# Kernel optimization log

Hardware: AMD Instinct MI355X
Metric: run time of the kernel (lower is better)

The kernel has to match this reference:

```python
import jax, jax.numpy as jnp
import numpy as np

B, D, H, O, E, K = 16384, 3072, 128, 10, 8, 2


def setup_inputs() -> dict:
    key = jax.random.key(0)
    ks = jax.random.split(key, 9)
    s_d = 1.0 / np.sqrt(D)
    s_h = 1.0 / np.sqrt(H)
    return {
        "x": jax.random.normal(ks[0], (B, D), dtype=jnp.float32),
        "gate_w": jax.random.uniform(ks[1], (D, E), jnp.float32, -s_d, s_d),
        "gate_b": jnp.zeros((E,), jnp.float32),
        "w1": jax.random.uniform(ks[2], (E, D, H), jnp.float32, -s_d, s_d),
        "b1": jax.random.uniform(ks[3], (E, H), jnp.float32, -s_d, s_d),
        "w2": jax.random.uniform(ks[4], (E, H, H), jnp.float32, -s_h, s_h),
        "b2": jax.random.uniform(ks[5], (E, H), jnp.float32, -s_h, s_h),
        "w3": jax.random.uniform(ks[6], (E, H, O), jnp.float32, -s_h, s_h),
        "b3": jax.random.uniform(ks[7], (E, O), jnp.float32, -s_h, s_h),
    }


def reference(x, gate_w, gate_b, w1, b1, w2, b2, w3, b3):
    # Gate: scores [B, E]
    scores = x @ gate_w + gate_b
    _, topk_idx = jax.lax.top_k(scores, K)          # [B, K]
    mask = jax.nn.one_hot(topk_idx, E, dtype=scores.dtype).sum(axis=-2)  # [B, E] 0/1
    weights = jax.nn.softmax(scores, axis=-1) * mask
    weights = weights / (weights.sum(axis=-1, keepdims=True) + 1e-8)

    # Compute all experts (dropout is identity in eval mode)
    h1 = jax.nn.relu(jnp.einsum('bd,edh->beh', x, w1) + b1)   # [B, E, H]
    h2 = jax.nn.relu(jnp.einsum('beh,ehg->beg', h1, w2) + b2)  # [B, E, H]
    out = jnp.einsum('beh,eho->beo', h2, w3) + b3              # [B, E, O]

    y = jnp.einsum('be,beo->bo', weights, out)                 # [B, O]
    return y
```

## Files before the change

### kernel.cpp

```cpp
#include <hip/hip_runtime.h>
#include <hip/hip_bf16.h>

#define B_ROWS 16384
#define D_DIM  3072
#define H_DIM  128
#define O_DIM  10
#define E_NUM  8

typedef __hip_bfloat16 bf16;
typedef __attribute__((ext_vector_type(8))) short short8;
typedef __attribute__((ext_vector_type(4))) float floatx4;

__device__ __forceinline__ void async_load16(const bf16* g, bf16* l) {
    __builtin_amdgcn_global_load_lds(
        (const __attribute__((address_space(1))) unsigned int*)(const void*)g,
        (__attribute__((address_space(3))) unsigned int*)(void*)l, 16, 0, 0);
}

__global__ void transpose_bf16_kernel(const float* __restrict__ in,
                                      bf16* __restrict__ out, int R, int C) {
    int e = blockIdx.z;
    const float* inp = in + (size_t)e * R * C;
    bf16* outp = out + (size_t)e * R * C;
    __shared__ float tile[32][33];
    int tx = threadIdx.x;
    int ty = threadIdx.y;
    int r0 = blockIdx.x * 32, c0 = blockIdx.y * 32;
#pragma unroll
    for (int i = 0; i < 4; i++)
        tile[ty + i * 8][tx] = inp[(size_t)(r0 + ty + i * 8) * C + c0 + tx];
    __syncthreads();
#pragma unroll
    for (int i = 0; i < 4; i++)
        outp[(size_t)(c0 + ty + i * 8) * R + r0 + tx] =
            __float2bfloat16(tile[tx][ty + i * 8]);
}

__global__ __launch_bounds__(256) void gate_w_reorder_kernel(
    const float* __restrict__ gw, float* __restrict__ gwr)
{
    int tid = blockIdx.x * 256 + threadIdx.x;
    int j = tid >> 9, rem = tid & 511;
    int k = rem >> 6, l = rem & 63;
    float4 v = *(const float4*)&gw[(size_t)(j * 256 + l * 4) * 8 + k * 4];
    *(float4*)&gwr[(size_t)tid * 4] = v;
}

__global__ __launch_bounds__(256, 4) void gate_kernel(
    const float* __restrict__ x, const float* __restrict__ gwr,
    const float* __restrict__ gate_b, bf16* __restrict__ x_bf16,
    int* __restrict__ rowlist, float* __restrict__ wlist, int* __restrict__ gcnt)
{
    __shared__ int   eidx[8][2];
    __shared__ float ew[8][2];
    __shared__ int   lcnt[E_NUM], gbase[E_NUM];

    int t = threadIdx.x, w = t >> 6, l = t & 63;
    int rowblk = blockIdx.x * 8;
    int r0 = rowblk + w * 2;

    float4 accA[2], accB[2];
#pragma unroll
    for (int r = 0; r < 2; r++) {
        accA[r] = (float4){0.f, 0.f, 0.f, 0.f};
        accB[r] = (float4){0.f, 0.f, 0.f, 0.f};
    }

    const float* xr0 = x + (size_t)r0 * D_DIM;
    const float* xr1 = x + (size_t)(r0 + 1) * D_DIM;
    int dl = l * 4;

    float4 xv[2], xn[2];
    xv[0] = *(const float4*)&xr0[dl];
    xv[1] = *(const float4*)&xr1[dl];

#pragma unroll 1
    for (int j = 0; j < 12; j++) {
        int dd = j * 256 + dl;
        const float4* gwp = (const float4*)(gwr + (size_t)j * 2048 + dl);
        float4 g[8];
#pragma unroll
        for (int k = 0; k < 8; k++) g[k] = gwp[k * 64];
        if (j < 11) {
            xn[0] = *(const float4*)&xr0[dd + 256];
            xn[1] = *(const float4*)&xr1[dd + 256];
        }
#pragma unroll
        for (int r = 0; r < 2; r++) {
            float4 xvv = xv[r];
            size_t xi = (size_t)(r0 + r) * D_DIM + dd;
            union { bf16 h[4]; uint2 v; } pk;
            pk.h[0] = __float2bfloat16(xvv.x);
            pk.h[1] = __float2bfloat16(xvv.y);
            pk.h[2] = __float2bfloat16(xvv.z);
            pk.h[3] = __float2bfloat16(xvv.w);
            *(uint2*)&x_bf16[xi] = pk.v;
            accA[r].x += xvv.x * g[0].x + xvv.y * g[2].x + xvv.z * g[4].x + xvv.w * g[6].x;
            accA[r].y += xvv.x * g[0].y + xvv.y * g[2].y + xvv.z * g[4].y + xvv.w * g[6].y;
            accA[r].z += xvv.x * g[0].z + xvv.y * g[2].z + xvv.z * g[4].z + xvv.w * g[6].z;
            accA[r].w += xvv.x * g[0].w + xvv.y * g[2].w + xvv.z * g[4].w + xvv.w * g[6].w;
            accB[r].x += xvv.x * g[1].x + xvv.y * g[3].x + xvv.z * g[5].x + xvv.w * g[7].x;
            accB[r].y += xvv.x * g[1].y + xvv.y * g[3].y + xvv.z * g[5].y + xvv.w * g[7].y;
            accB[r].z += xvv.x * g[1].z + xvv.y * g[3].z + xvv.z * g[5].z + xvv.w * g[7].z;
            accB[r].w += xvv.x * g[1].w + xvv.y * g[3].w + xvv.z * g[5].w + xvv.w * g[7].w;
        }
        xv[0] = xn[0];
        xv[1] = xn[1];
    }

#pragma unroll
    for (int r = 0; r < 2; r++) {
        float s[8] = {accA[r].x, accA[r].y, accA[r].z, accA[r].w,
                      accB[r].x, accB[r].y, accB[r].z, accB[r].w};
#pragma unroll
        for (int e = 0; e < 8; e++) {
            float v = s[e];
#pragma unroll
            for (int off = 1; off < 64; off <<= 1) v += __shfl_xor(v, off, 64);
            s[e] = v;
        }
        accA[r] = (float4){s[0], s[1], s[2], s[3]};
        accB[r] = (float4){s[4], s[5], s[6], s[7]};
    }

    if (l == 0) {
#pragma unroll
        for (int r = 0; r < 2; r++) {
            float s[8] = {accA[r].x, accA[r].y, accA[r].z, accA[r].w,
                          accB[r].x, accB[r].y, accB[r].z, accB[r].w};
#pragma unroll
            for (int e = 0; e < 8; e++) s[e] += gate_b[e];
            int i1 = 0; float m1 = s[0];
#pragma unroll
            for (int e = 1; e < 8; e++) if (s[e] > m1) { m1 = s[e]; i1 = e; }
            int i2 = -1; float m2 = -1e30f;
#pragma unroll
            for (int e = 0; e < 8; e++)
                if (e != i1 && s[e] > m2) { m2 = s[e]; i2 = e; }
            float S = 0.0f;
#pragma unroll
            for (int e = 0; e < 8; e++) S += expf(s[e] - m1);
            float p1 = expf(s[i1] - m1) / S;
            float p2 = expf(m2 - m1) / S;
            float denom = p1 + p2 + 1e-8f;
            eidx[w * 2 + r][0] = i1; ew[w * 2 + r][0] = p1 / denom;
            eidx[w * 2 + r][1] = i2; ew[w * 2 + r][1] = p2 / denom;
        }
    }
    __syncthreads();
    if (t < 8) lcnt[t] = 0;
    __syncthreads();
    int my_e = 0, my_lp = 0, my_rl = 0, my_sl = 0;
    if (t < 16) {
        my_rl = t >> 1; my_sl = t & 1;
        my_e = eidx[my_rl][my_sl];
        my_lp = atomicAdd(&lcnt[my_e], 1);
    }
    __syncthreads();
    if (t < 8) gbase[t] = atomicAdd(&gcnt[t], lcnt[t]);
    __syncthreads();
    if (t < 16) {
        int pos = gbase[my_e] + my_lp;
        rowlist[my_e * B_ROWS + pos] = rowblk + my_rl;
        wlist[my_e * B_ROWS + pos]   = ew[my_rl][my_sl];
    }
}

__global__ __launch_bounds__(512, 4) void gemm1_kernel(
    const bf16* __restrict__ xb, const bf16* __restrict__ w1t,
    const float* __restrict__ b1, const int* __restrict__ rowlist,
    const int* __restrict__ gcnt, bf16* __restrict__ h1buf)
{
    int e  = blockIdx.x & 7;
    int bx = blockIdx.x >> 3;
    int cnt = gcnt[e];
    int t0 = bx * 128;
    if (t0 >= cnt) return;
    int mcnt = cnt - t0; if (mcnt > 128) mcnt = 128;

    __shared__ bf16 Ab[2][128 * 64];
    __shared__ bf16 Bb[2][128 * 64];
    __shared__ int rows_s[128];

    int t = threadIdx.x, w = t >> 6, l = t & 63;
    if (t < 128) {
        int rr = (t < mcnt) ? t : (mcnt - 1);
        rows_s[t] = rowlist[e * B_ROWS + t0 + rr];
    }
    __syncthreads();

    const bf16* w1base = w1t + (size_t)e * H_DIM * D_DIM;
    int sub = l >> 3;
    int blk = (l & 7) ^ sub;
    const bf16* aP0 = xb + (size_t)rows_s[w * 16 + sub]     * D_DIM + blk * 8;
    const bf16* aP1 = xb + (size_t)rows_s[w * 16 + 8 + sub] * D_DIM + blk * 8;
    const bf16* bP0 = w1base + (size_t)(w * 16 + sub)     * D_DIM + blk * 8;
    const bf16* bP1 = w1base + (size_t)(w * 16 + 8 + sub) * D_DIM + blk * 8;
    bf16* ldsA0 = &Ab[0][(2 * w) * 512], *ldsA1 = &Ab[0][(2 * w + 1) * 512];
    bf16* ldsB0 = &Bb[0][(2 * w) * 512], *ldsB1 = &Bb[0][(2 * w + 1) * 512];

    auto stage = [&](int bs, int kb) {
        int k0 = kb * 64;
        int boff = bs * 128 * 64;
        async_load16(aP0 + k0, ldsA0 + boff);
        async_load16(aP1 + k0, ldsA1 + boff);
        async_load16(bP0 + k0, ldsB0 + boff);
        async_load16(bP1 + k0, ldsB1 + boff);
    };

    int wr = w & 3, wc = w >> 2;
    floatx4 acc[2][4];
#pragma unroll
    for (int mi = 0; mi < 2; mi++)
#pragma unroll
        for (int ni = 0; ni < 4; ni++) acc[mi][ni] = (floatx4){0.f, 0.f, 0.f, 0.f};

    stage(0, 0);

    const int NKB = D_DIM / 64;
    for (int kb = 0; kb < NKB; kb++) {
        int bs = kb & 1;
        __syncthreads();
        if (kb + 1 < NKB) stage(bs ^ 1, kb + 1);
#pragma unroll
        for (int kc8 = 0; kc8 < 8; kc8 += 4) {
            int c = kc8 + (l >> 4);
            int swz = (c ^ (l & 7)) * 8;
            short8 af[2], bfr[4];
#pragma unroll
            for (int mi = 0; mi < 2; mi++) {
                int R = wr * 32 + mi * 16 + (l & 15);
                af[mi] = *(const short8*)&Ab[bs][R * 64 + swz];
            }
#pragma unroll
            for (int ni = 0; ni < 4; ni++) {
                int C = wc * 64 + ni * 16 + (l & 15);
                bfr[ni] = *(const short8*)&Bb[bs][C * 64 + swz];
            }
#pragma unroll
            for (int mi = 0; mi < 2; mi++)
#pragma unroll
                for (int ni = 0; ni < 4; ni++)
                    acc[mi][ni] = __builtin_amdgcn_mfma_f32_16x16x32_bf16(
                        af[mi], bfr[ni], acc[mi][ni], 0, 0, 0);
        }
    }

    const float* b1e = b1 + e * H_DIM;
#pragma unroll
    for (int mi = 0; mi < 2; mi++)
#pragma unroll
        for (int r = 0; r < 4; r++) {
            int row = wr * 32 + mi * 16 + (l >> 4) * 4 + r;
            if (row < mcnt) {
#pragma unroll
                for (int ni = 0; ni < 4; ni++) {
                    int col = wc * 64 + ni * 16 + (l & 15);
                    float v = fmaxf(acc[mi][ni][r] + b1e[col], 0.0f);
                    h1buf[(size_t)e * B_ROWS * H_DIM + (size_t)(t0 + row) * H_DIM + col] =
                        __float2bfloat16(v);
                }
            }
        }
}

__global__ __launch_bounds__(256) void gemm2c_kernel(
    const bf16* __restrict__ h1buf, const bf16* __restrict__ w2t,
    const float* __restrict__ b2, const float* __restrict__ w3,
    const float* __restrict__ b3, const int* __restrict__ rowlist,
    const float* __restrict__ wlist, const int* __restrict__ gcnt,
    float* __restrict__ y)
{
    int e  = blockIdx.x & 7;
    int bx = blockIdx.x >> 3;
    int cnt = gcnt[e];
    int t0 = bx * 64;
    if (t0 >= cnt) return;
    int mcnt = cnt - t0; if (mcnt > 64) mcnt = 64;

    __shared__ bf16 h1s[64][136];
    __shared__ bf16 w2s[128][136];
    __shared__ bf16 w3ts[16 * 136];
    __shared__ float b2s[H_DIM], b3s[16], wts[64];
    __shared__ int rows_s[64];

    int t = threadIdx.x, w = t >> 6, l = t & 63;

    if (t < 64) {
        int rr = (t < mcnt) ? t : (mcnt - 1);
        rows_s[t] = rowlist[e * B_ROWS + t0 + rr];
        wts[t]    = wlist[e * B_ROWS + t0 + rr];
    }
    if (t < H_DIM) b2s[t] = b2[e * H_DIM + t];
    if (t < O_DIM) b3s[t] = b3[e * O_DIM + t];
    for (int idx = t; idx < H_DIM * O_DIM; idx += 256)
        w3ts[(idx % 10) * 136 + idx / 10] = __float2bfloat16(w3[(size_t)e * H_DIM * O_DIM + idx]);
    for (int idx = t; idx < 6 * 128; idx += 256)
        w3ts[(10 + idx / 128) * 136 + (idx % 128)] = __float2bfloat16(0.0f);

    {
        const bf16* h1base = h1buf + (size_t)e * B_ROWS * H_DIM + (size_t)t0 * H_DIM;
        int hend = mcnt * 16;
#pragma unroll
        for (int k = 0; k < 4; k++) {
            int si = t + 256 * k;
            if (si < hend)
                *(uint4*)&h1s[si >> 4][(si & 15) * 8] =
                    *(const uint4*)(h1base + (size_t)(si >> 4) * H_DIM + (si & 15) * 8);
        }
        const bf16* w2base = w2t + (size_t)e * H_DIM * H_DIM;
#pragma unroll
        for (int k = 0; k < 8; k++) {
            int si = t + 256 * k;
            *(uint4*)&w2s[si >> 4][(si & 15) * 8] =
                *(const uint4*)(w2base + (size_t)(si >> 4) * H_DIM + (si & 15) * 8);
        }
    }
    __syncthreads();

    int mb = (w & 1) * 32, nb = (w >> 1) * 64;
    floatx4 acc2[2][4];
#pragma unroll
    for (int mi = 0; mi < 2; mi++)
#pragma unroll
        for (int ni = 0; ni < 4; ni++) acc2[mi][ni] = (floatx4){0.f, 0.f, 0.f, 0.f};
#pragma unroll
    for (int kc = 0; kc < 128; kc += 32) {
        short8 af[2], bfr[4];
#pragma unroll
        for (int mi = 0; mi < 2; mi++)
            af[mi] = *(const short8*)&h1s[mb + mi * 16 + (l & 15)][kc + (l >> 4) * 8];
#pragma unroll
        for (int ni = 0; ni < 4; ni++)
            bfr[ni] = *(const short8*)&w2s[nb + ni * 16 + (l & 15)][kc + (l >> 4) * 8];
#pragma unroll
        for (int mi = 0; mi < 2; mi++)
#pragma unroll
            for (int ni = 0; ni < 4; ni++)
                acc2[mi][ni] = __builtin_amdgcn_mfma_f32_16x16x32_bf16(
                    af[mi], bfr[ni], acc2[mi][ni], 0, 0, 0);
    }
    __syncthreads();

    bf16* h2s = &h1s[0][0];
#pragma unroll
    for (int mi = 0; mi < 2; mi++)
#pragma unroll
        for (int r = 0; r < 4; r++) {
            int row = mb + mi * 16 + (l >> 4) * 4 + r;
#pragma unroll
            for (int ni = 0; ni < 4; ni++) {
                int col = nb + ni * 16 + (l & 15);
                float v = fmaxf(acc2[mi][ni][r] + b2s[col], 0.0f);
                h2s[row * 136 + col] = __float2bfloat16(v);
            }
        }
    __syncthreads();

    floatx4 acc3 = (floatx4){0.f, 0.f, 0.f, 0.f};
    int m3 = w * 16;
#pragma unroll
    for (int kc = 0; kc < 128; kc += 32) {
        short8 af  = *(const short8*)&h2s[(m3 + (l & 15)) * 136 + kc + (l >> 4) * 8];
        short8 bf3 = *(const short8*)&w3ts[(l & 15) * 136 + kc + (l >> 4) * 8];
        acc3 = __builtin_amdgcn_mfma_f32_16x16x32_bf16(af, bf3, acc3, 0, 0, 0);
    }
    int col = l & 15;
    if (col < O_DIM) {
#pragma unroll
        for (int r = 0; r < 4; r++) {
            int row = m3 + (l >> 4) * 4 + r;
            if (row < mcnt)
                atomicAdd(&y[(size_t)rows_s[row] * O_DIM + col],
                          wts[row] * (acc3[r] + b3s[col]));
        }
    }
}

extern "C" void kernel_launch(void* const* d_in, const int* in_sizes, int n_in,
                              void* d_out, int out_size, void* d_ws, size_t ws_size,
                              hipStream_t stream) {
    (void)in_sizes; (void)n_in; (void)ws_size;
    const float* x      = (const float*)d_in[0];
    const float* gate_w = (const float*)d_in[1];
    const float* gate_b = (const float*)d_in[2];
    const float* w1     = (const float*)d_in[3];
    const float* b1     = (const float*)d_in[4];
    const float* w2     = (const float*)d_in[5];
    const float* b2     = (const float*)d_in[6];
    const float* w3     = (const float*)d_in[7];
    const float* b3     = (const float*)d_in[8];
    float* y = (float*)d_out;

    char* ws = (char*)d_ws;
    size_t off = 0;
    auto alloc = [&](size_t bytes) {
        void* p = ws + off;
        off = (off + bytes + 255) & ~(size_t)255;
        return p;
    };
    bf16*  x_bf16  = (bf16*)alloc((size_t)B_ROWS * D_DIM * 2);
    bf16*  w1t     = (bf16*)alloc((size_t)E_NUM * H_DIM * D_DIM * 2);
    bf16*  w2t     = (bf16*)alloc((size_t)E_NUM * H_DIM * H_DIM * 2);
    bf16*  h1buf   = (bf16*)alloc((size_t)E_NUM * B_ROWS * H_DIM * 2);
    float* gwr     = (float*)alloc((size_t)D_DIM * E_NUM * 4);
    int*   rowlist = (int*)alloc((size_t)E_NUM * B_ROWS * 4);
    float* wlist   = (float*)alloc((size_t)E_NUM * B_ROWS * 4);
    int*   gcnt    = (int*)alloc(64);

    hipMemsetAsync(d_out, 0, (size_t)out_size * sizeof(float), stream);
    hipMemsetAsync(gcnt, 0, 64, stream);

    gate_w_reorder_kernel<<<D_DIM * E_NUM / 4 / 256, 256, 0, stream>>>(gate_w, gwr);
    transpose_bf16_kernel<<<dim3(D_DIM / 32, H_DIM / 32, E_NUM), dim3(32, 8), 0, stream>>>(
        w1, w1t, D_DIM, H_DIM);
    transpose_bf16_kernel<<<dim3(H_DIM / 32, H_DIM / 32, E_NUM), dim3(32, 8), 0, stream>>>(
        w2, w2t, H_DIM, H_DIM);
    gate_kernel<<<B_ROWS / 8, 256, 0, stream>>>(x, gwr, gate_b, x_bf16,
                                                rowlist, wlist, gcnt);
    gemm1_kernel<<<(B_ROWS / 128) * E_NUM, 512, 0, stream>>>(
        x_bf16, w1t, b1, rowlist, gcnt, h1buf);
    gemm2c_kernel<<<(B_ROWS / 64) * E_NUM, 256, 0, stream>>>(
        h1buf, w2t, b2, w3, b3, rowlist, wlist, gcnt, y);
}
```

Baseline: 428.7 us.

## Fuse expert GEMM1 with GEMM2/GEMM3 keeping h1 in LDS; deepen gate prefetch

Merges the first expert GEMM with the second/third GEMM and weighted scatter into one kernel, so the ReLU'd h1 tile stays in shared memory instead of round-tripping through a global buffer. It removes one kernel launch and the h1 global write/read. The gate kernel gets a two-step-ahead x prefetch and a higher occupancy hint. The fused kernel uses more LDS per block, which may reduce resident blocks per CU.

```diff
diff --git a/kernel.cpp b/kernel.cpp
--- a/kernel.cpp
+++ b/kernel.cpp
@@ -46,7 +46,7 @@
     *(float4*)&gwr[(size_t)tid * 4] = v;
 }
 
-__global__ __launch_bounds__(256, 4) void gate_kernel(
+__global__ __launch_bounds__(256, 8) void gate_kernel(
     const float* __restrict__ x, const float* __restrict__ gwr,
     const float* __restrict__ gate_b, bf16* __restrict__ x_bf16,
     int* __restrict__ rowlist, float* __restrict__ wlist, int* __restrict__ gcnt)
@@ -73,6 +73,8 @@
     float4 xv[2], xn[2];
     xv[0] = *(const float4*)&xr0[dl];
     xv[1] = *(const float4*)&xr1[dl];
+    xn[0] = *(const float4*)&xr0[dl + 256];
+    xn[1] = *(const float4*)&xr1[dl + 256];
 
 #pragma unroll 1
     for (int j = 0; j < 12; j++) {
@@ -81,9 +83,10 @@
         float4 g[8];
 #pragma unroll
         for (int k = 0; k < 8; k++) g[k] = gwp[k * 64];
-        if (j < 11) {
-            xn[0] = *(const float4*)&xr0[dd + 256];
-            xn[1] = *(const float4*)&xr1[dd + 256];
+        float4 xm0 = xn[0], xm1 = xn[1];
+        if (j < 10) {
+            xm0 = *(const float4*)&xr0[dd + 512];
+            xm1 = *(const float4*)&xr1[dd + 512];
         }
 #pragma unroll
         for (int r = 0; r < 2; r++) {
@@ -104,8 +107,8 @@
             accB[r].z += xvv.x * g[1].z + xvv.y * g[3].z + xvv.z * g[5].z + xvv.w * g[7].z;
             accB[r].w += xvv.x * g[1].w + xvv.y * g[3].w + xvv.z * g[5].w + xvv.w * g[7].w;
         }
-        xv[0] = xn[0];
-        xv[1] = xn[1];
+        xv[0] = xn[0]; xv[1] = xn[1];
+        xn[0] = xm0;   xn[1] = xm1;
     }
 
 #pragma unroll
@@ -166,10 +169,13 @@
     }
 }
 
-__global__ __launch_bounds__(512, 4) void gemm1_kernel(
+__global__ __launch_bounds__(512, 4) void moe_fused_kernel(
     const bf16* __restrict__ xb, const bf16* __restrict__ w1t,
-    const float* __restrict__ b1, const int* __restrict__ rowlist,
-    const int* __restrict__ gcnt, bf16* __restrict__ h1buf)
+    const float* __restrict__ b1, const bf16* __restrict__ w2t,
+    const float* __restrict__ b2, const float* __restrict__ w3,
+    const float* __restrict__ b3, const int* __restrict__ rowlist,
+    const float* __restrict__ wlist, const int* __restrict__ gcnt,
+    float* __restrict__ y)
 {
     int e  = blockIdx.x & 7;
     int bx = blockIdx.x >> 3;
@@ -178,14 +184,25 @@
     if (t0 >= cnt) return;
     int mcnt = cnt - t0; if (mcnt > 128) mcnt = 128;
 
-    __shared__ bf16 Ab[2][128 * 64];
-    __shared__ bf16 Bb[2][128 * 64];
-    __shared__ int rows_s[128];
+    __shared__ __align__(16) char smem[73984];
+    __shared__ int   rows_s[128];
+    __shared__ float wts[128];
+    __shared__ float b1s[H_DIM], b2s[H_DIM], b3s[O_DIM];
+
+    bf16* AbP = (bf16*)smem;
+    bf16* BbP = (bf16*)(smem + 32768);
 
     int t = threadIdx.x, w = t >> 6, l = t & 63;
     if (t < 128) {
         int rr = (t < mcnt) ? t : (mcnt - 1);
         rows_s[t] = rowlist[e * B_ROWS + t0 + rr];
+        wts[t]    = wlist[e * B_ROWS + t0 + rr];
+    } else if (t < 256) {
+        b1s[t - 128] = b1[e * H_DIM + (t - 128)];
+    } else if (t < 384) {
+        b2s[t - 256] = b2[e * H_DIM + (t - 256)];
+    } else if (t < 384 + O_DIM) {
+        b3s[t - 384] = b3[e * O_DIM + (t - 384)];
     }
     __syncthreads();
 
@@ -196,8 +213,8 @@
     const bf16* aP1 = xb + (size_t)rows_s[w * 16 + 8 + sub] * D_DIM + blk * 8;
     const bf16* bP0 = w1base + (size_t)(w * 16 + sub)     * D_DIM + blk * 8;
     const bf16* bP1 = w1base + (size_t)(w * 16 + 8 + sub) * D_DIM + blk * 8;
-    bf16* ldsA0 = &Ab[0][(2 * w) * 512], *ldsA1 = &Ab[0][(2 * w + 1) * 512];
-    bf16* ldsB0 = &Bb[0][(2 * w) * 512], *ldsB1 = &Bb[0][(2 * w + 1) * 512];
+    bf16* ldsA0 = AbP + (2 * w) * 512, *ldsA1 = AbP + (2 * w + 1) * 512;
+    bf16* ldsB0 = BbP + (2 * w) * 512, *ldsB1 = BbP + (2 * w + 1) * 512;
 
     auto stage = [&](int bs, int kb) {
         int k0 = kb * 64;
@@ -230,12 +247,12 @@
 #pragma unroll
             for (int mi = 0; mi < 2; mi++) {
                 int R = wr * 32 + mi * 16 + (l & 15);
-                af[mi] = *(const short8*)&Ab[bs][R * 64 + swz];
+                af[mi] = *(const short8*)&AbP[bs * 8192 + R * 64 + swz];
             }
 #pragma unroll
             for (int ni = 0; ni < 4; ni++) {
                 int C = wc * 64 + ni * 16 + (l & 15);
-                bfr[ni] = *(const short8*)&Bb[bs][C * 64 + swz];
+                bfr[ni] = *(const short8*)&BbP[bs * 8192 + C * 64 + swz];
             }
 #pragma unroll
             for (int mi = 0; mi < 2; mi++)
@@ -245,80 +262,42 @@
                         af[mi], bfr[ni], acc[mi][ni], 0, 0, 0);
         }
     }
-
-    const float* b1e = b1 + e * H_DIM;
+    __syncthreads();
+
+    bf16* h1s  = (bf16*)smem;
+    bf16* w2s  = (bf16*)(smem + 34816);
+    bf16* w3ts = (bf16*)(smem + 69632);
+
 #pragma unroll
     for (int mi = 0; mi < 2; mi++)
 #pragma unroll
         for (int r = 0; r < 4; r++) {
             int row = wr * 32 + mi * 16 + (l >> 4) * 4 + r;
-            if (row < mcnt) {
-#pragma unroll
-                for (int ni = 0; ni < 4; ni++) {
-                    int col = wc * 64 + ni * 16 + (l & 15);
-                    float v = fmaxf(acc[mi][ni][r] + b1e[col], 0.0f);
-                    h1buf[(size_t)e * B_ROWS * H_DIM + (size_t)(t0 + row) * H_DIM + col] =
-                        __float2bfloat16(v);
-                }
+#pragma unroll
+            for (int ni = 0; ni < 4; ni++) {
+                int col = wc * 64 + ni * 16 + (l & 15);
+                h1s[row * 136 + col] =
+                    __float2bfloat16(fmaxf(acc[mi][ni][r] + b1s[col], 0.0f));
             }
         }
-}
-
-__global__ __launch_bounds__(256) void gemm2c_kernel(
-    const bf16* __restrict__ h1buf, const bf16* __restrict__ w2t,
-    const float* __restrict__ b2, const float* __restrict__ w3,
-    const float* __restrict__ b3, const int* __restrict__ rowlist,
-    const float* __restrict__ wlist, const int* __restrict__ gcnt,
-    float* __restrict__ y)
-{
-    int e  = blockIdx.x & 7;
-    int bx = blockIdx.x >> 3;
-    int cnt = gcnt[e];
-    int t0 = bx * 64;
-    if (t0 >= cnt) return;
-    int mcnt = cnt - t0; if (mcnt > 64) mcnt = 64;
-
-    __shared__ bf16 h1s[64][136];
-    __shared__ bf16 w2s[128][136];
-    __shared__ bf16 w3ts[16 * 136];
-    __shared__ float b2s[H_DIM], b3s[16], wts[64];
-    __shared__ int rows_s[64];
-
-    int t = threadIdx.x, w = t >> 6, l = t & 63;
-
-    if (t < 64) {
-        int rr = (t < mcnt) ? t : (mcnt - 1);
-        rows_s[t] = rowlist[e * B_ROWS + t0 + rr];
-        wts[t]    = wlist[e * B_ROWS + t0 + rr];
-    }
-    if (t < H_DIM) b2s[t] = b2[e * H_DIM + t];
-    if (t < O_DIM) b3s[t] = b3[e * O_DIM + t];
-    for (int idx = t; idx < H_DIM * O_DIM; idx += 256)
-        w3ts[(idx % 10) * 136 + idx / 10] = __float2bfloat16(w3[(size_t)e * H_DIM * O_DIM + idx]);
-    for (int idx = t; idx < 6 * 128; idx += 256)
-        w3ts[(10 + idx / 128) * 136 + (idx % 128)] = __float2bfloat16(0.0f);
 
     {
-        const bf16* h1base = h1buf + (size_t)e * B_ROWS * H_DIM + (size_t)t0 * H_DIM;
-        int hend = mcnt * 16;
+        const bf16* w2base = w2t + (size_t)e * H_DIM * H_DIM;
 #pragma unroll
         for (int k = 0; k < 4; k++) {
-            int si = t + 256 * k;
-            if (si < hend)
-                *(uint4*)&h1s[si >> 4][(si & 15) * 8] =
-                    *(const uint4*)(h1base + (size_t)(si >> 4) * H_DIM + (si & 15) * 8);
-        }
-        const bf16* w2base = w2t + (size_t)e * H_DIM * H_DIM;
-#pragma unroll
-        for (int k = 0; k < 8; k++) {
-            int si = t + 256 * k;
-            *(uint4*)&w2s[si >> 4][(si & 15) * 8] =
+            int si = t + 512 * k;
+            *(uint4*)&w2s[(si >> 4) * 136 + (si & 15) * 8] =
                 *(const uint4*)(w2base + (size_t)(si >> 4) * H_DIM + (si & 15) * 8);
         }
-    }
-    __syncthreads();
-
-    int mb = (w & 1) * 32, nb = (w >> 1) * 64;
+        for (int idx = t; idx < H_DIM * O_DIM; idx += 512)
+            w3ts[(idx % 10) * 136 + idx / 10] =
+                __float2bfloat16(w3[(size_t)e * H_DIM * O_DIM + idx]);
+        for (int idx = t; idx < 6 * 128; idx += 512)
+            w3ts[(10 + idx / 128) * 136 + (idx % 128)] = __float2bfloat16(0.0f);
+    }
+    __syncthreads();
+
+    int mb = wr * 32, nb = wc * 64;
     floatx4 acc2[2][4];
 #pragma unroll
     for (int mi = 0; mi < 2; mi++)
@@ -329,10 +308,10 @@
         short8 af[2], bfr[4];
 #pragma unroll
         for (int mi = 0; mi < 2; mi++)
-            af[mi] = *(const short8*)&h1s[mb + mi * 16 + (l & 15)][kc + (l >> 4) * 8];
+            af[mi] = *(const short8*)&h1s[(mb + mi * 16 + (l & 15)) * 136 + kc + (l >> 4) * 8];
 #pragma unroll
         for (int ni = 0; ni < 4; ni++)
-            bfr[ni] = *(const short8*)&w2s[nb + ni * 16 + (l & 15)][kc + (l >> 4) * 8];
+            bfr[ni] = *(const short8*)&w2s[(nb + ni * 16 + (l & 15)) * 136 + kc + (l >> 4) * 8];
 #pragma unroll
         for (int mi = 0; mi < 2; mi++)
 #pragma unroll
@@ -342,7 +321,7 @@
     }
     __syncthreads();
 
-    bf16* h2s = &h1s[0][0];
+    bf16* h2s = h1s;
 #pragma unroll
     for (int mi = 0; mi < 2; mi++)
 #pragma unroll
@@ -351,8 +330,8 @@
 #pragma unroll
             for (int ni = 0; ni < 4; ni++) {
                 int col = nb + ni * 16 + (l & 15);
-                float v = fmaxf(acc2[mi][ni][r] + b2s[col], 0.0f);
-                h2s[row * 136 + col] = __float2bfloat16(v);
+                h2s[row * 136 + col] =
+                    __float2bfloat16(fmaxf(acc2[mi][ni][r] + b2s[col], 0.0f));
             }
         }
     __syncthreads();
@@ -402,7 +381,6 @@
     bf16*  x_bf16  = (bf16*)alloc((size_t)B_ROWS * D_DIM * 2);
     bf16*  w1t     = (bf16*)alloc((size_t)E_NUM * H_DIM * D_DIM * 2);
     bf16*  w2t     = (bf16*)alloc((size_t)E_NUM * H_DIM * H_DIM * 2);
-    bf16*  h1buf   = (bf16*)alloc((size_t)E_NUM * B_ROWS * H_DIM * 2);
     float* gwr     = (float*)alloc((size_t)D_DIM * E_NUM * 4);
     int*   rowlist = (int*)alloc((size_t)E_NUM * B_ROWS * 4);
     float* wlist   = (float*)alloc((size_t)E_NUM * B_ROWS * 4);
@@ -418,8 +396,6 @@
         w2, w2t, H_DIM, H_DIM);
     gate_kernel<<<B_ROWS / 8, 256, 0, stream>>>(x, gwr, gate_b, x_bf16,
                                                 rowlist, wlist, gcnt);
-    gemm1_kernel<<<(B_ROWS / 128) * E_NUM, 512, 0, stream>>>(
-        x_bf16, w1t, b1, rowlist, gcnt, h1buf);
-    gemm2c_kernel<<<(B_ROWS / 64) * E_NUM, 256, 0, stream>>>(
-        h1buf, w2t, b2, w3, b3, rowlist, wlist, gcnt, y);
-}
+    moe_fused_kernel<<<(B_ROWS / 128) * E_NUM, 512, 0, stream>>>(
+        x_bf16, w1t, b1, w2t, b2, w3, b3, rowlist, wlist, gcnt, y);
+}
```

After: 631.4 us. 1.47x slower.
